# Performance work log

Measured on AMD Instinct MI355X. Metric: run time of the kernel, lower is better.

Reference implementation:

```python
import jax, jax.numpy as jnp
import numpy as np

B, T, U = 64, 800, 80          # batch, stroke timesteps, char sequence length
IN, H, V = 3, 400, 57          # input_dim, hidden_dim, onehot_dim (vocab)
K, G = 10, 20                  # n_window, n_gaussian
D1 = H + IN + V                # input dim of recurrent layers >= 1


def setup_inputs() -> dict:
    key = jax.random.key(0)
    ks = jax.random.split(key, 12)
    std = 0.075
    nrm = lambda k, shp: (std * jax.random.normal(k, shp)).astype(jnp.float32)
    char_ids = jax.random.randint(ks[1], (B, U), 0, V)
    return {
        "x_input": jax.random.normal(ks[0], (B, T, IN), jnp.float32),
        "onehot": jax.nn.one_hot(char_ids, V, dtype=jnp.float32),
        "h0": jnp.zeros((B, H), jnp.float32),
        "h1": jnp.zeros((B, H), jnp.float32),
        "h2": jnp.zeros((B, H), jnp.float32),
        # GRU layer 0 (input: strokes only)
        "W_ih0": nrm(ks[2], (3 * H, IN)), "W_hh0": nrm(ks[3], (3 * H, H)),
        "b_ih0": jnp.zeros((3 * H,), jnp.float32), "b_hh0": jnp.zeros((3 * H,), jnp.float32),
        # GRU layer 1 (shared by all layers >= 1, faithful to the torch code which
        # always calls self.rnn_layer1 in the loop)
        "W_ih1": nrm(ks[4], (3 * H, D1)), "W_hh1": nrm(ks[5], (3 * H, H)),
        "b_ih1": jnp.zeros((3 * H,), jnp.float32), "b_hh1": jnp.zeros((3 * H,), jnp.float32),
        # attention window linear: hidden -> 3*K (alpha, beta, kappa); bias ~ N(-4, 0.1)
        "W_win": nrm(ks[6], (3 * K, H)),
        "b_win": (-4.0 + 0.1 * jax.random.normal(ks[7], (3 * K,))).astype(jnp.float32),
        # MDN head: hidden -> 1 + 6*G
        "W_mdn": nrm(ks[8], (1 + 6 * G, H)),
        "b_mdn": jnp.zeros((1 + 6 * G,), jnp.float32),
    }


def gru(x, h0, W_ih, W_hh, b_ih, b_hh):
    """PyTorch-convention GRU. x: (B,T,D), h0: (B,H) -> (out (B,T,H), hT (B,H))."""
    xg = jnp.einsum('btd,gd->btg', x, W_ih) + b_ih  # (B,T,3H), precomputed input gates

    def step(h, xg_t):
        gh = h @ W_hh.T + b_hh
        xr, xz, xn = jnp.split(xg_t, 3, axis=-1)
        hr, hz, hn = jnp.split(gh, 3, axis=-1)
        r = jax.nn.sigmoid(xr + hr)
        z = jax.nn.sigmoid(xz + hz)
        n = jnp.tanh(xn + r * hn)
        h_new = (1.0 - z) * n + z * h
        return h_new, h_new

    hT, outs = jax.lax.scan(step, h0, jnp.swapaxes(xg, 0, 1))
    return jnp.swapaxes(outs, 0, 1), hT


def reference(x_input, onehot, h0, h1, h2,
              W_ih0, W_hh0, b_ih0, b_hh0,
              W_ih1, W_hh1, b_ih1, b_hh1,
              W_win, b_win, W_mdn, b_mdn):
    out0, _ = gru(x_input, h0, W_ih0, W_hh0, b_ih0, b_hh0)  # (B,T,H)

    # Graves attention window (training=True path: running_kappa = cumsum(kappa))
    abk = jnp.exp(out0 @ W_win.T + b_win)                    # (B,T,3K)
    alpha, beta, kappa = jnp.split(abk, 3, axis=-1)          # each (B,T,K)
    running_kappa = jnp.cumsum(kappa, axis=1)                # (B,T,K)
    u = jnp.arange(onehot.shape[1], dtype=x_input.dtype)     # (U,)
    diff = running_kappa[..., None] - u                      # (B,T,K,U)
    phi = jnp.sum(alpha[..., None] * jnp.exp(-beta[..., None] * diff * diff), axis=2)  # (B,T,U)
    window = jnp.einsum('btu,buv->btv', phi, onehot)         # (B,T,V)

    # layers >= 1 all use layer-1 weights (faithful to original torch code)
    out = jnp.concatenate([out0, window, x_input], axis=-1)
    out, _ = gru(out, h1, W_ih1, W_hh1, b_ih1, b_hh1)
    out = jnp.concatenate([out, window, x_input], axis=-1)
    out, _ = gru(out, h2, W_ih1, W_hh1, b_ih1, b_hh1)

    mdn = out.reshape(-1, H) @ W_mdn.T + b_mdn               # (B*T, 1+6G)
    pi_logit = mdn[:, 0 * G:1 * G]
    mu1 = mdn[:, 1 * G:2 * G]
    mu2 = mdn[:, 2 * G:3 * G]
    log_sigma1 = mdn[:, 3 * G:4 * G]
    log_sigma2 = mdn[:, 4 * G:5 * G]
    rho = jnp.tanh(mdn[:, 5 * G:6 * G])
    e_logit = mdn[:, 6 * G:]
    return jnp.concatenate([pi_logit, mu1, mu2, log_sigma1, log_sigma2, rho, e_logit], axis=-1)
```

## Files before the change

kernel.cpp:

```cpp
#include <hip/hip_runtime.h>
#include <math.h>

#define Bx 64
#define Tx 800
#define Ux 80
#define INx 3
#define Hx 400
#define Vx 57
#define Kx 10


typedef float v2f __attribute__((ext_vector_type(2)));
typedef float v4f __attribute__((ext_vector_type(4)));

__device__ __forceinline__ float sigf(float x) { return 1.f / (1.f + expf(-x)); }

__device__ __forceinline__ void pk_lo(v2f& acc, v2f w, v2f h) {
    asm("v_pk_fma_f32 %0, %1, %2, %0 op_sel:[0,0,0] op_sel_hi:[0,1,1]"
        : "+v"(acc) : "v"(w), "v"(h));
}
__device__ __forceinline__ void pk_hi(v2f& acc, v2f w, v2f h) {
    asm("v_pk_fma_f32 %0, %1, %2, %0 op_sel:[1,0,0] op_sel_hi:[1,1,1]"
        : "+v"(acc) : "v"(w), "v"(h));
}

__global__ void k_zero(int* __restrict__ cnt) {
    int i = blockIdx.x * blockDim.x + threadIdx.x;
    if (i < 3 * 16 * 32) cnt[i] = 0;
}

__global__ void k_transpose_x(const float* __restrict__ x, float* __restrict__ xT) {
    int idx = blockIdx.x * blockDim.x + threadIdx.x;
    if (idx >= Tx * INx * Bx) return;
    int b = idx & 63;
    int d = (idx >> 6) % INx;
    int t = idx / (64 * INx);
    xT[idx] = x[((size_t)b * Tx + t) * INx + d];
}

__global__ void k_transpose_oh(const float* __restrict__ oh, float* __restrict__ ohT) {
    int idx = blockIdx.x * blockDim.x + threadIdx.x;
    if (idx >= Ux * Vx * Bx) return;
    int b = idx & 63;
    int uv = idx >> 6;
    int v = uv % Vx;
    int u = uv / Vx;
    ohT[idx] = oh[((size_t)b * Ux + u) * Vx + v];
}

__global__ void k_packW(const float* __restrict__ Whh, const float* __restrict__ Wih,
                        float* __restrict__ Wp, int NP, int xcols) {
    int idx = blockIdx.x * blockDim.x + threadIdx.x;
    int total = 16 * 3 * NP * 400;
    if (idx >= total) return;
    int q = idx % 400;
    int m = (idx / 400) % (3 * NP);
    int us = idx / (400 * 3 * NP);
    int g = m / NP, p = m % NP;
    int s = q / 25, u = q % 25;
    int row = g * 400 + us * 25 + u;
    float v0, v1;
    if (p < 13) {
        int kl0 = 2 * p, kl1 = 2 * p + 1;
        v0 = (kl0 < 25) ? Whh[(size_t)row * 400 + s * 25 + kl0] : 0.f;
        v1 = (kl1 < 25) ? Whh[(size_t)row * 400 + s * 25 + kl1] : 0.f;
    } else {
        int jx0 = 2 * (p - 13), jx1 = jx0 + 1;
        int kx0 = s * 29 + jx0, kx1 = s * 29 + jx1;
        v0 = (jx0 < 29 && kx0 < xcols) ? Wih[(size_t)row * xcols + kx0] : 0.f;
        v1 = (jx1 < 29 && kx1 < xcols) ? Wih[(size_t)row * xcols + kx1] : 0.f;
    }
    Wp[(size_t)idx * 2]     = v0;
    Wp[(size_t)idx * 2 + 1] = v1;
}

template <int XP>
__global__ __launch_bounds__(448, 1) void k_rec(
    const float* __restrict__ Wp, const float* __restrict__ prev,
    const float* __restrict__ winb, const float* __restrict__ xT,
    const float* __restrict__ hinit, const float* __restrict__ Wih_small,
    const float* __restrict__ bih, const float* __restrict__ bhh,
    float* __restrict__ outL, int* __restrict__ cnt) {
    constexpr int NP = 13 + XP;
    constexpr int XW = (XP > 0) ? 466 : 4;
    __shared__ __align__(16) float xcat_h[404 * 4];
    __shared__ __align__(16) float xcat_x[2][XW * 4];
    __shared__ __align__(16) float hprev[2][104 * 4];
    __shared__ v2f red2[8 * 400];
    __shared__ float biasLDS[150];
    __shared__ float wih0LDS[225];

    const int tid = threadIdx.x;
    const int us = blockIdx.x >> 4;
    const int cg = blockIdx.x & 15;
    const int cb = cg * 4;
    const int U0 = us * 25;
    const int q = tid;
    const int s = q / 25;
    int* cnt_cg = cnt + cg * 32;

    v2f w[3 * NP];
    if (q < 400) {
        const v2f* Wp2 = (const v2f*)Wp;
        #pragma unroll
        for (int m = 0; m < 3 * NP; ++m)
            w[m] = Wp2[((size_t)(us * 3 * NP) + m) * 400 + q];
    } else {
        #pragma unroll
        for (int m = 0; m < 3 * NP; ++m) w[m] = (v2f){0.f, 0.f};
    }
    if (tid < 75)        biasLDS[tid] = bih[(tid / 25) * 400 + U0 + (tid % 25)];
    else if (tid < 150)  biasLDS[tid] = bhh[((tid - 75) / 25) * 400 + U0 + ((tid - 75) % 25)];
    if (XP == 0 && tid < 225) {
        int u = tid / 9, r9 = tid % 9, g = r9 / 3, d = r9 % 3;
        wih0LDS[tid] = Wih_small[(size_t)(g * 400 + U0 + u) * 3 + d];
    }
    for (int k = tid; k < 404; k += 448)
        *(v4f*)&xcat_h[k * 4] = (v4f){0.f, 0.f, 0.f, 0.f};
    for (int k = tid; k < 2 * XW; k += 448)
        *(v4f*)&xcat_x[0][k * 4] = (v4f){0.f, 0.f, 0.f, 0.f};

    if (XP > 0) {
        for (int kx = tid; kx < 460; kx += 448) {
            v4f xv;
            if (kx < 400)      xv = *(const v4f*)(prev + (size_t)kx * 64 + cb);
            else if (kx < 457) xv = *(const v4f*)(winb + (size_t)(kx - 400) * 64 + cb);
            else               xv = *(const v4f*)(xT + (size_t)(kx - 457) * 64 + cb);
            *(v4f*)&xcat_x[0][kx * 4] = xv;
        }
    } else {
        if (tid < 3)
            *(v4f*)&xcat_x[0][tid * 4] = *(const v4f*)(xT + (size_t)tid * 64 + cb);
    }

    for (int t = 0; t < Tx; ++t) {
        const int pl = t & 1;
        if (t > 0) {
            int* fp = cnt_cg + (tid & 31);
            int fv = __hip_atomic_load(fp, __ATOMIC_RELAXED, __HIP_MEMORY_SCOPE_AGENT);
            while (!__all(fv >= t)) {
                __builtin_amdgcn_s_sleep(1);
                fv = __hip_atomic_load(fp, __ATOMIC_RELAXED, __HIP_MEMORY_SCOPE_AGENT);
            }
        }
        if (tid < 400) {
            v4f hv;
            if (t == 0) {
                hv.x = hinit[(size_t)(cb + 0) * 400 + tid];
                hv.y = hinit[(size_t)(cb + 1) * 400 + tid];
                hv.z = hinit[(size_t)(cb + 2) * 400 + tid];
                hv.w = hinit[(size_t)(cb + 3) * 400 + tid];
            } else {
                const float* hp0 = outL + (size_t)(t - 1) * 25600 + (size_t)tid * 64 + cb;
                asm volatile("global_load_dwordx4 %0, %1, off sc0 sc1"
                             : "=v"(hv) : "v"(hp0) : "memory");
                asm volatile("s_waitcnt vmcnt(0)" ::: "memory");
            }
            *(v4f*)&xcat_h[tid * 4] = hv;
            int d = tid - U0;
            if ((unsigned)d < 25u) *(v4f*)&hprev[t & 1][d * 4] = hv;
        }
        __syncthreads();

        if (q < 400) {
            v2f aR0 = {0, 0}, aR1 = {0, 0}, aZ0 = {0, 0}, aZ1 = {0, 0};
            v2f aHN0 = {0, 0}, aHN1 = {0, 0}, aXN0 = {0, 0}, aXN1 = {0, 0};
            const float* hb = &xcat_h[s * 100];
            #pragma unroll
            for (int p = 0; p < 13; ++p) {
                v2f a01 = *(const v2f*)(hb + 8 * p);
                v2f a23 = *(const v2f*)(hb + 8 * p + 2);
                v2f b01 = *(const v2f*)(hb + 8 * p + 4);
                v2f b23 = *(const v2f*)(hb + 8 * p + 6);
                v2f wr = w[p], wz = w[NP + p], wn = w[2 * NP + p];
                pk_lo(aR0, wr, a01);  pk_lo(aR1, wr, a23);
                pk_hi(aR0, wr, b01);  pk_hi(aR1, wr, b23);
                pk_lo(aZ0, wz, a01);  pk_lo(aZ1, wz, a23);
                pk_hi(aZ0, wz, b01);  pk_hi(aZ1, wz, b23);
                pk_lo(aHN0, wn, a01); pk_lo(aHN1, wn, a23);
                pk_hi(aHN0, wn, b01); pk_hi(aHN1, wn, b23);
            }
            if (XP > 0) {
                const float* xb = &xcat_x[pl][s * 29 * 4];
                #pragma unroll
                for (int p = 0; p < XP; ++p) {
                    v2f a01 = *(const v2f*)(xb + 8 * p);
                    v2f a23 = *(const v2f*)(xb + 8 * p + 2);
                    v2f b01 = *(const v2f*)(xb + 8 * p + 4);
                    v2f b23 = *(const v2f*)(xb + 8 * p + 6);
                    v2f wr = w[13 + p], wz = w[NP + 13 + p], wn = w[2 * NP + 13 + p];
                    pk_lo(aR0, wr, a01);  pk_lo(aR1, wr, a23);
                    pk_hi(aR0, wr, b01);  pk_hi(aR1, wr, b23);
                    pk_lo(aZ0, wz, a01);  pk_lo(aZ1, wz, a23);
                    pk_hi(aZ0, wz, b01);  pk_hi(aZ1, wz, b23);
                    pk_lo(aXN0, wn, a01); pk_lo(aXN1, wn, a23);
                    pk_hi(aXN0, wn, b01); pk_hi(aXN1, wn, b23);
                }
            }
            red2[0 * 400 + q] = aR0;  red2[1 * 400 + q] = aR1;
            red2[2 * 400 + q] = aZ0;  red2[3 * 400 + q] = aZ1;
            red2[4 * 400 + q] = aHN0; red2[5 * 400 + q] = aHN1;
            red2[6 * 400 + q] = aXN0; red2[7 * 400 + q] = aXN1;
        }
        __syncthreads();

        if (tid < 128) {
            if (tid < 100) {
                int u = tid >> 2, c = tid & 3;
                int half = c >> 1, e = c & 1;
                const float* redf = (const float*)red2;
                float R = 0, Z = 0, HN = 0, XN = 0;
                #pragma unroll 4
                for (int s2 = 0; s2 < 16; ++s2) {
                    int idx = s2 * 25 + u;
                    R  += redf[((0 + half) * 400 + idx) * 2 + e];
                    Z  += redf[((2 + half) * 400 + idx) * 2 + e];
                    HN += redf[((4 + half) * 400 + idx) * 2 + e];
                    XN += redf[((6 + half) * 400 + idx) * 2 + e];
                }
                R += biasLDS[u] + biasLDS[75 + u];
                Z += biasLDS[25 + u] + biasLDS[100 + u];
                XN += biasLDS[50 + u];
                HN += biasLDS[125 + u];
                if (XP == 0) {
                    #pragma unroll
                    for (int d = 0; d < 3; ++d) {
                        float xv = xcat_x[pl][d * 4 + c];
                        R  += wih0LDS[u * 9 + 0 + d] * xv;
                        Z  += wih0LDS[u * 9 + 3 + d] * xv;
                        XN += wih0LDS[u * 9 + 6 + d] * xv;
                    }
                }
                float r = sigf(R);
                float z = sigf(Z);
                float n = tanhf(XN + r * HN);
                float hp = hprev[t & 1][u * 4 + c];
                float hnew = (1.f - z) * n + z * hp;
                __hip_atomic_store(outL + (size_t)t * 25600 + (size_t)(U0 + u) * 64 + cb + c,
                                   hnew, __ATOMIC_RELAXED, __HIP_MEMORY_SCOPE_AGENT);
            }
            asm volatile("s_waitcnt vmcnt(0)" ::: "memory");
            if ((tid & 63) == 0)
                __hip_atomic_store(cnt_cg + us * 2 + (tid >> 6), t + 1,
                                   __ATOMIC_RELAXED, __HIP_MEMORY_SCOPE_AGENT);
        } else if (t + 1 < Tx) {
            const int p2 = (t + 1) & 1;
            if (XP > 0) {
                for (int kx = tid - 128; kx < 460; kx += 320) {
                    v4f xv;
                    if (kx < 400)      xv = *(const v4f*)(prev + (size_t)(t + 1) * 25600 + kx * 64 + cb);
                    else if (kx < 457) xv = *(const v4f*)(winb + (size_t)(t + 1) * 3648 + (kx - 400) * 64 + cb);
                    else               xv = *(const v4f*)(xT + (size_t)(t + 1) * 192 + (kx - 457) * 64 + cb);
                    *(v4f*)&xcat_x[p2][kx * 4] = xv;
                }
            } else {
                if (tid < 131) {
                    int d = tid - 128;
                    *(v4f*)&xcat_x[p2][d * 4] = *(const v4f*)(xT + (size_t)(t + 1) * 192 + d * 64 + cb);
                }
            }
        }
    }
}

__global__ __launch_bounds__(256) void k_abk(const float* __restrict__ out0,
    const float* __restrict__ Wwin, const float* __restrict__ bwin,
    float* __restrict__ abk) {
    int t = blockIdx.x;
    int b = threadIdx.x & 63;
    int js = threadIdx.x >> 6;
    int j0 = js * 8;
    int nj = min(8, 30 - j0);
    float acc[8];
    for (int i = 0; i < nj; i++) acc[i] = bwin[j0 + i];
    const float* o = out0 + (size_t)t * 25600;
    for (int k = 0; k < Hx; k++) {
        float hv = o[k * 64 + b];
        for (int i = 0; i < nj; i++) acc[i] += Wwin[(j0 + i) * Hx + k] * hv;
    }
    for (int i = 0; i < nj; i++)
        abk[(size_t)t * 1920 + (j0 + i) * 64 + b] = expf(acc[i]);
}

__global__ void k_cumsum(float* __restrict__ abk) {
    int tid = blockIdx.x * blockDim.x + threadIdx.x;
    if (tid >= Kx * Bx) return;
    int b = tid & 63;
    int k = tid >> 6;
    float run = 0.f;
    size_t base = (size_t)(20 + k) * 64 + b;
    for (int t = 0; t < Tx; t++) {
        size_t i = (size_t)t * 1920 + base;
        run += abk[i];
        abk[i] = run;
    }
}

__global__ __launch_bounds__(256) void k_window(const float* __restrict__ abk,
    const float* __restrict__ ohT, float* __restrict__ win) {
    int t = blockIdx.x;
    int b = threadIdx.x & 63;
    int sub = threadIdx.x >> 6;
    __shared__ float phi[Ux][64];

    float al[Kx], be[Kx], kc[Kx];
    const float* ab = abk + (size_t)t * 1920;
    #pragma unroll
    for (int k = 0; k < Kx; k++) {
        al[k] = ab[k * 64 + b];
        be[k] = ab[(10 + k) * 64 + b];
        kc[k] = ab[(20 + k) * 64 + b];
    }
    for (int u = sub * 20; u < sub * 20 + 20; u++) {
        float ssum = 0.f;
        float uf = (float)u;
        #pragma unroll
        for (int k = 0; k < Kx; k++) {
            float d = kc[k] - uf;
            ssum += al[k] * __expf(-be[k] * d * d);
        }
        phi[u][b] = ssum;
    }
    __syncthreads();

    int v0 = sub * 15;
    int nv = min(15, Vx - v0);
    float acc[15];
    for (int i = 0; i < nv; i++) acc[i] = 0.f;
    for (int u = 0; u < Ux; u++) {
        float pv = phi[u][b];
        const float* oh = ohT + (size_t)(u * Vx) * 64;
        for (int i = 0; i < nv; i++) acc[i] += pv * oh[(v0 + i) * 64 + b];
    }
    for (int i = 0; i < nv; i++)
        win[(size_t)t * 3648 + (v0 + i) * 64 + b] = acc[i];
}

__global__ __launch_bounds__(256) void k_mdn(const float* __restrict__ out2,
    const float* __restrict__ Wm, const float* __restrict__ bm,
    float* __restrict__ out) {
    int t = blockIdx.x;
    int b = threadIdx.x & 63;
    int js = threadIdx.x >> 6;
    int j0 = js * 31;
    int nj = min(31, 121 - j0);
    float acc[31];
    for (int i = 0; i < nj; i++) acc[i] = bm[j0 + i];
    const float* o = out2 + (size_t)t * 25600;
    for (int k = 0; k < Hx; k += 4) {
        float i0 = o[k * 64 + b];
        float i1 = o[(k + 1) * 64 + b];
        float i2 = o[(k + 2) * 64 + b];
        float i3 = o[(k + 3) * 64 + b];
        for (int i = 0; i < nj; i++) {
            const float* wp = Wm + (size_t)(j0 + i) * Hx + k;
            float4 qv = *(const float4*)wp;
            acc[i] += qv.x * i0 + qv.y * i1 + qv.z * i2 + qv.w * i3;
        }
    }
    size_t rb = ((size_t)b * Tx + t) * 121;
    for (int i = 0; i < nj; i++) {
        int j = j0 + i;
        float v = acc[i];
        if (j >= 100 && j < 120) v = tanhf(v);
        out[rb + j] = v;
    }
}

extern "C" void kernel_launch(void* const* d_in, const int* in_sizes, int n_in,
                              void* d_out, int out_size, void* d_ws, size_t ws_size,
                              hipStream_t stream) {
    const float* x    = (const float*)d_in[0];
    const float* oneh = (const float*)d_in[1];
    const float* h0i  = (const float*)d_in[2];
    const float* h1i  = (const float*)d_in[3];
    const float* h2i  = (const float*)d_in[4];
    const float* Wih0 = (const float*)d_in[5];
    const float* Whh0 = (const float*)d_in[6];
    const float* bih0 = (const float*)d_in[7];
    const float* bhh0 = (const float*)d_in[8];
    const float* Wih1 = (const float*)d_in[9];
    const float* Whh1 = (const float*)d_in[10];
    const float* bih1 = (const float*)d_in[11];
    const float* bhh1 = (const float*)d_in[12];
    const float* Wwin = (const float*)d_in[13];
    const float* bwin = (const float*)d_in[14];
    const float* Wmdn = (const float*)d_in[15];
    const float* bmdn = (const float*)d_in[16];

    float* ws    = (float*)d_ws;
    float* out0  = ws;
    float* out12 = ws + 20480000;
    float* winb  = ws + 40960000;
    float* abk   = ws + 43878400;
    float* xT    = ws + 45414400;
    float* ohT   = ws + 45568000;
    float* Wp0   = ws + 45859840;
    float* Wp12  = ws + 46359040;
    int*   cnt   = (int*)(ws + 47434240);

    hipLaunchKernelGGL(k_zero, dim3(6), dim3(256), 0, stream, cnt);
    hipLaunchKernelGGL(k_transpose_x, dim3((Tx * INx * Bx + 255) / 256), dim3(256), 0, stream, x, xT);
    hipLaunchKernelGGL(k_transpose_oh, dim3((Ux * Vx * Bx + 255) / 256), dim3(256), 0, stream, oneh, ohT);
    hipLaunchKernelGGL(k_packW, dim3((16 * 3 * 13 * 400 + 255) / 256), dim3(256), 0, stream,
                       Whh0, Wih0, Wp0, 13, 3);
    hipLaunchKernelGGL(k_packW, dim3((16 * 3 * 28 * 400 + 255) / 256), dim3(256), 0, stream,
                       Whh1, Wih1, Wp12, 28, 460);

    hipLaunchKernelGGL((k_rec<0>), dim3(256), dim3(448), 0, stream,
                       Wp0, (const float*)nullptr, (const float*)nullptr, xT,
                       h0i, Wih0, bih0, bhh0, out0, cnt + 0 * 512);

    hipLaunchKernelGGL(k_abk, dim3(Tx), dim3(256), 0, stream, out0, Wwin, bwin, abk);
    hipLaunchKernelGGL(k_cumsum, dim3(10), dim3(64), 0, stream, abk);
    hipLaunchKernelGGL(k_window, dim3(Tx), dim3(256), 0, stream, abk, ohT, winb);

    hipLaunchKernelGGL((k_rec<15>), dim3(256), dim3(448), 0, stream,
                       Wp12, out0, winb, xT, h1i, (const float*)nullptr,
                       bih1, bhh1, out12, cnt + 1 * 512);
    hipLaunchKernelGGL((k_rec<15>), dim3(256), dim3(448), 0, stream,
                       Wp12, out12, winb, xT, h2i, (const float*)nullptr,
                       bih1, bhh1, out0, cnt + 2 * 512);

    hipLaunchKernelGGL(k_mdn, dim3(Tx), dim3(256), 0, stream, out0, Wmdn, bmdn, (float*)d_out);
}
```

Before: 16.38 ms.

## Poll step flags from one wavefront and reduce gates in a single wave

Only the first wavefront now spins on the cross-block step counters, and the other waves wait at a block barrier, so the whole block no longer polls global memory. The gate reduction runs on one 64-thread wave covering the 100 outputs in two passes, which leaves one flag per block instead of two and cuts the flags each poller checks from 32 to 16. The weight register array is split into per-gate arrays. The trade is an extra barrier per timestep and a longer serial reduction inside one wave, which sits on the recurrent critical path.

```diff
diff --git a/kernel.cpp b/kernel.cpp
--- a/kernel.cpp
+++ b/kernel.cpp
@@ -99,15 +99,21 @@
     const int s = q / 25;
     int* cnt_cg = cnt + cg * 32;
 
-    v2f w[3 * NP];
+    v2f wr[NP], wz[NP], wn[NP];
     if (q < 400) {
         const v2f* Wp2 = (const v2f*)Wp;
+        const size_t base = (size_t)(us * 3 * NP) * 400 + q;
         #pragma unroll
-        for (int m = 0; m < 3 * NP; ++m)
-            w[m] = Wp2[((size_t)(us * 3 * NP) + m) * 400 + q];
+        for (int m = 0; m < NP; ++m) {
+            wr[m] = Wp2[base + (size_t)m * 400];
+            wz[m] = Wp2[base + (size_t)(NP + m) * 400];
+            wn[m] = Wp2[base + (size_t)(2 * NP + m) * 400];
+        }
     } else {
         #pragma unroll
-        for (int m = 0; m < 3 * NP; ++m) w[m] = (v2f){0.f, 0.f};
+        for (int m = 0; m < NP; ++m) {
+            wr[m] = (v2f){0.f, 0.f}; wz[m] = (v2f){0.f, 0.f}; wn[m] = (v2f){0.f, 0.f};
+        }
     }
     if (tid < 75)        biasLDS[tid] = bih[(tid / 25) * 400 + U0 + (tid % 25)];
     else if (tid < 150)  biasLDS[tid] = bhh[((tid - 75) / 25) * 400 + U0 + ((tid - 75) % 25)];
@@ -136,12 +142,15 @@
     for (int t = 0; t < Tx; ++t) {
         const int pl = t & 1;
         if (t > 0) {
-            int* fp = cnt_cg + (tid & 31);
-            int fv = __hip_atomic_load(fp, __ATOMIC_RELAXED, __HIP_MEMORY_SCOPE_AGENT);
-            while (!__all(fv >= t)) {
-                __builtin_amdgcn_s_sleep(1);
-                fv = __hip_atomic_load(fp, __ATOMIC_RELAXED, __HIP_MEMORY_SCOPE_AGENT);
-            }
+            if (tid < 64) {
+                int* fp = cnt_cg + (tid & 15);
+                int fv = __hip_atomic_load(fp, __ATOMIC_RELAXED, __HIP_MEMORY_SCOPE_AGENT);
+                while (!__all(fv >= t)) {
+                    __builtin_amdgcn_s_sleep(1);
+                    fv = __hip_atomic_load(fp, __ATOMIC_RELAXED, __HIP_MEMORY_SCOPE_AGENT);
+                }
+            }
+            __syncthreads();
         }
         if (tid < 400) {
             v4f hv;
@@ -172,13 +181,13 @@
                 v2f a23 = *(const v2f*)(hb + 8 * p + 2);
                 v2f b01 = *(const v2f*)(hb + 8 * p + 4);
                 v2f b23 = *(const v2f*)(hb + 8 * p + 6);
-                v2f wr = w[p], wz = w[NP + p], wn = w[2 * NP + p];
-                pk_lo(aR0, wr, a01);  pk_lo(aR1, wr, a23);
-                pk_hi(aR0, wr, b01);  pk_hi(aR1, wr, b23);
-                pk_lo(aZ0, wz, a01);  pk_lo(aZ1, wz, a23);
-                pk_hi(aZ0, wz, b01);  pk_hi(aZ1, wz, b23);
-                pk_lo(aHN0, wn, a01); pk_lo(aHN1, wn, a23);
-                pk_hi(aHN0, wn, b01); pk_hi(aHN1, wn, b23);
+                v2f r_ = wr[p], z_ = wz[p], n_ = wn[p];
+                pk_lo(aR0, r_, a01);  pk_lo(aR1, r_, a23);
+                pk_hi(aR0, r_, b01);  pk_hi(aR1, r_, b23);
+                pk_lo(aZ0, z_, a01);  pk_lo(aZ1, z_, a23);
+                pk_hi(aZ0, z_, b01);  pk_hi(aZ1, z_, b23);
+                pk_lo(aHN0, n_, a01); pk_lo(aHN1, n_, a23);
+                pk_hi(aHN0, n_, b01); pk_hi(aHN1, n_, b23);
             }
             if (XP > 0) {
                 const float* xb = &xcat_x[pl][s * 29 * 4];
@@ -188,13 +197,13 @@
                     v2f a23 = *(const v2f*)(xb + 8 * p + 2);
                     v2f b01 = *(const v2f*)(xb + 8 * p + 4);
                     v2f b23 = *(const v2f*)(xb + 8 * p + 6);
-                    v2f wr = w[13 + p], wz = w[NP + 13 + p], wn = w[2 * NP + 13 + p];
-                    pk_lo(aR0, wr, a01);  pk_lo(aR1, wr, a23);
-                    pk_hi(aR0, wr, b01);  pk_hi(aR1, wr, b23);
-                    pk_lo(aZ0, wz, a01);  pk_lo(aZ1, wz, a23);
-                    pk_hi(aZ0, wz, b01);  pk_hi(aZ1, wz, b23);
-                    pk_lo(aXN0, wn, a01); pk_lo(aXN1, wn, a23);
-                    pk_hi(aXN0, wn, b01); pk_hi(aXN1, wn, b23);
+                    v2f r_ = wr[13 + p], z_ = wz[13 + p], n_ = wn[13 + p];
+                    pk_lo(aR0, r_, a01);  pk_lo(aR1, r_, a23);
+                    pk_hi(aR0, r_, b01);  pk_hi(aR1, r_, b23);
+                    pk_lo(aZ0, z_, a01);  pk_lo(aZ1, z_, a23);
+                    pk_hi(aZ0, z_, b01);  pk_hi(aZ1, z_, b23);
+                    pk_lo(aXN0, n_, a01); pk_lo(aXN1, n_, a23);
+                    pk_hi(aXN0, n_, b01); pk_hi(aXN1, n_, b23);
                 }
             }
             red2[0 * 400 + q] = aR0;  red2[1 * 400 + q] = aR1;
@@ -204,49 +213,53 @@
         }
         __syncthreads();
 
-        if (tid < 128) {
-            if (tid < 100) {
-                int u = tid >> 2, c = tid & 3;
-                int half = c >> 1, e = c & 1;
-                const float* redf = (const float*)red2;
-                float R = 0, Z = 0, HN = 0, XN = 0;
-                #pragma unroll 4
-                for (int s2 = 0; s2 < 16; ++s2) {
-                    int idx = s2 * 25 + u;
-                    R  += redf[((0 + half) * 400 + idx) * 2 + e];
-                    Z  += redf[((2 + half) * 400 + idx) * 2 + e];
-                    HN += redf[((4 + half) * 400 + idx) * 2 + e];
-                    XN += redf[((6 + half) * 400 + idx) * 2 + e];
+        if (tid < 64) {
+            #pragma unroll
+            for (int rep = 0; rep < 2; ++rep) {
+                int o = tid + rep * 64;
+                if (o < 100) {
+                    int u = o >> 2, c = o & 3;
+                    int half = c >> 1, e = c & 1;
+                    const float* redf = (const float*)red2;
+                    float R = 0, Z = 0, HN = 0, XN = 0;
+                    #pragma unroll 4
+                    for (int s2 = 0; s2 < 16; ++s2) {
+                        int idx = s2 * 25 + u;
+                        R  += redf[((0 + half) * 400 + idx) * 2 + e];
+                        Z  += redf[((2 + half) * 400 + idx) * 2 + e];
+                        HN += redf[((4 + half) * 400 + idx) * 2 + e];
+                        XN += redf[((6 + half) * 400 + idx) * 2 + e];
+                    }
+                    R += biasLDS[u] + biasLDS[75 + u];
+                    Z += biasLDS[25 + u] + biasLDS[100 + u];
+                    XN += biasLDS[50 + u];
+                    HN += biasLDS[125 + u];
+                    if (XP == 0) {
+                        #pragma unroll
+                        for (int d = 0; d < 3; ++d) {
+                            float xv = xcat_x[pl][d * 4 + c];
+                            R  += wih0LDS[u * 9 + 0 + d] * xv;
+                            Z  += wih0LDS[u * 9 + 3 + d] * xv;
+                            XN += wih0LDS[u * 9 + 6 + d] * xv;
+                        }
+                    }
+                    float r = sigf(R);
+                    float z = sigf(Z);
+                    float n = tanhf(XN + r * HN);
+                    float hp = hprev[t & 1][u * 4 + c];
+                    float hnew = (1.f - z) * n + z * hp;
+                    __hip_atomic_store(outL + (size_t)t * 25600 + (size_t)(U0 + u) * 64 + cb + c,
+                                       hnew, __ATOMIC_RELAXED, __HIP_MEMORY_SCOPE_AGENT);
                 }
-                R += biasLDS[u] + biasLDS[75 + u];
-                Z += biasLDS[25 + u] + biasLDS[100 + u];
-                XN += biasLDS[50 + u];
-                HN += biasLDS[125 + u];
-                if (XP == 0) {
-                    #pragma unroll
-                    for (int d = 0; d < 3; ++d) {
-                        float xv = xcat_x[pl][d * 4 + c];
-                        R  += wih0LDS[u * 9 + 0 + d] * xv;
-                        Z  += wih0LDS[u * 9 + 3 + d] * xv;
-                        XN += wih0LDS[u * 9 + 6 + d] * xv;
-                    }
-                }
-                float r = sigf(R);
-                float z = sigf(Z);
-                float n = tanhf(XN + r * HN);
-                float hp = hprev[t & 1][u * 4 + c];
-                float hnew = (1.f - z) * n + z * hp;
-                __hip_atomic_store(outL + (size_t)t * 25600 + (size_t)(U0 + u) * 64 + cb + c,
-                                   hnew, __ATOMIC_RELAXED, __HIP_MEMORY_SCOPE_AGENT);
             }
             asm volatile("s_waitcnt vmcnt(0)" ::: "memory");
-            if ((tid & 63) == 0)
-                __hip_atomic_store(cnt_cg + us * 2 + (tid >> 6), t + 1,
+            if (tid == 0)
+                __hip_atomic_store(cnt_cg + us, t + 1,
                                    __ATOMIC_RELAXED, __HIP_MEMORY_SCOPE_AGENT);
         } else if (t + 1 < Tx) {
             const int p2 = (t + 1) & 1;
             if (XP > 0) {
-                for (int kx = tid - 128; kx < 460; kx += 320) {
+                for (int kx = tid - 64; kx < 460; kx += 384) {
                     v4f xv;
                     if (kx < 400)      xv = *(const v4f*)(prev + (size_t)(t + 1) * 25600 + kx * 64 + cb);
                     else if (kx < 457) xv = *(const v4f*)(winb + (size_t)(t + 1) * 3648 + (kx - 400) * 64 + cb);
@@ -254,8 +267,8 @@
                     *(v4f*)&xcat_x[p2][kx * 4] = xv;
                 }
             } else {
-                if (tid < 131) {
-                    int d = tid - 128;
+                if (tid < 67) {
+                    int d = tid - 64;
                     *(v4f*)&xcat_x[p2][d * 4] = *(const v4f*)(xT + (size_t)(t + 1) * 192 + d * 64 + cb);
                 }
             }
```

Measured after the change: 13.78 ms. 15.9% less time.
